# Performance work log

Measured on AMD Instinct MI355X. Metric: run time of the kernel, lower is better.

Reference implementation:

```python
import jax, jax.numpy as jnp
import numpy as np

N = 300000
MAX_TORSION = 7
MAX_RIGID = 8
MAX_SS = 3
MAX_ATOM = 24
NRES = 22
EPS = 1e-6


def v_norm_safe(v):
    # normalize last dim with epsilon clamp (torch v_norm_safe analogue)
    return v / jnp.clip(jnp.linalg.norm(v, axis=-1, keepdims=True), EPS)


def combine_operations(X, Y):
    # X, Y: [..., 4, 3] rigid ops (3x3 rotation rows + 1 translation row)
    rot = X[..., :3, :] @ Y[..., :3, :]
    t = jnp.einsum('...ij,...j->...i', X[..., :3, :], Y[..., 3, :]) + X[..., 3, :]
    return jnp.concatenate([rot, t[..., None, :]], axis=-2)


def setup_inputs() -> dict:
    key = jax.random.key(0)
    ks = jax.random.split(key, 9)
    return {
        'output_0': jax.random.normal(ks[0], (N, 2 * MAX_TORSION + MAX_SS, 1), jnp.float32),
        'output_1': jax.random.normal(ks[1], (N, 3, 3), jnp.float32),
        'pos': jax.random.normal(ks[2], (N, 3), jnp.float32),
        'ss': jax.random.randint(ks[3], (N,), 0, MAX_SS),
        'residue_type': jax.random.randint(ks[4], (N,), 0, NRES),
        'rigid_transforms': jax.random.normal(ks[5], (MAX_SS, NRES, MAX_RIGID, 4, 3), jnp.float32),
        'rigid_groups': jax.random.normal(ks[6], (MAX_SS, NRES, MAX_ATOM, 3), jnp.float32),
        'transforms_dep': jax.random.randint(ks[7], (NRES, MAX_RIGID), 0, MAX_RIGID),
        'rigids_dep': jax.random.randint(ks[8], (NRES, MAX_ATOM), 0, MAX_RIGID),
    }


def reference(output_0, output_1, pos, ss, residue_type,
              rigid_transforms, rigid_groups, transforms_dep, rigids_dep):
    # ---- StructureModule.output_to_opr_6D ----
    bb0 = output_1[:, :2]                                   # [N,2,3]
    e0 = v_norm_safe(bb0[:, 0])
    v1 = bb0[:, 1]
    u1 = v1 - e0 * jnp.sum(e0 * v1, axis=-1, keepdims=True)
    e1 = v_norm_safe(u1)
    e2 = jnp.cross(e0, e1)
    rot = jnp.stack([e0, e1, e2], axis=1).swapaxes(-1, -2)  # [N,3,3]
    t = 0.1 * output_1[:, 2][:, None, :]                    # [N,1,3]
    bb = jnp.concatenate([rot, t], axis=1)                  # [N,4,3]
    sc = v_norm_safe(output_0[:, :2 * MAX_TORSION].reshape(-1, MAX_TORSION, 2))

    # ---- build_structure ----
    transforms = rigid_transforms[ss, residue_type]         # [N,8,4,3]
    rigids = rigid_groups[ss, residue_type]                 # [N,24,3]
    tdep = transforms_dep[residue_type]                     # [N,8]
    rdep = rigids_dep[residue_type]                         # [N,24]

    n = output_0.shape[0]
    c, s = sc[..., 0], sc[..., 1]                           # [N,7]
    zr = jnp.zeros_like(c)
    on = jnp.ones_like(c)
    tor_rot = jnp.stack([
        jnp.stack([on, zr, zr], axis=-1),
        jnp.stack([zr, c, -s], axis=-1),
        jnp.stack([zr, s, c], axis=-1),
    ], axis=-2)                                             # [N,7,3,3]
    tor = jnp.concatenate(
        [tor_rot, jnp.zeros((n, MAX_TORSION, 1, 3), output_0.dtype)], axis=2)
    opr0 = jnp.concatenate([bb[:, :3], (bb[:, 3] + pos)[:, None]], axis=1)  # [N,4,3]
    opr = jnp.concatenate([opr0[:, None], tor], axis=1)     # [N,8,4,3]

    opr = combine_operations(transforms, opr)
    for i_tor in range(1, MAX_RIGID):                       # fixed 7-step dependency chain
        prev = jnp.take_along_axis(opr, tdep[:, i_tor][:, None, None, None], axis=1)[:, 0]
        opr = opr.at[:, i_tor].set(combine_operations(prev, opr[:, i_tor]))

    opr_g = jnp.take_along_axis(opr, rdep[:, :, None, None], axis=1)  # [N,24,4,3]
    R = jnp.einsum('naij,naj->nai', opr_g[:, :, :3], rigids) + opr_g[:, :, 3]
    return (R, opr[:, 0])
```

## Files before the change

### kernel.cpp

```cpp
#include <hip/hip_runtime.h>
#include <math.h>

#define NRES 22


__device__ __forceinline__ void sel8(const float (&fr)[8][12], int d, float (&P)[12]) {
    const bool b0 = (d & 1) != 0;
    const bool b1 = (d & 2) != 0;
    const bool b2 = (d & 4) != 0;
#pragma unroll
    for (int k = 0; k < 12; ++k) {
        float a01 = b0 ? fr[1][k] : fr[0][k];
        float a23 = b0 ? fr[3][k] : fr[2][k];
        float a45 = b0 ? fr[5][k] : fr[4][k];
        float a67 = b0 ? fr[7][k] : fr[6][k];
        float b03 = b1 ? a23 : a01;
        float b47 = b1 ? a67 : a45;
        P[k] = b2 ? b47 : b03;
    }
}

__device__ __forceinline__ void apply_point(const float (&F)[12], float x, float y, float z,
                                            float &px, float &py, float &pz) {
    px = fmaf(F[0], x, fmaf(F[1], y, fmaf(F[2], z, F[9])));
    py = fmaf(F[3], x, fmaf(F[4], y, fmaf(F[5], z, F[10])));
    pz = fmaf(F[6], x, fmaf(F[7], y, fmaf(F[8], z, F[11])));
}

extern "C" __global__ __launch_bounds__(256)
void model_kernel(const float* __restrict__ o0,
                  const float* __restrict__ o1,
                  const float* __restrict__ pos,
                  const int*   __restrict__ ssArr,
                  const int*   __restrict__ rtArr,
                  const float* __restrict__ rigT,
                  const float* __restrict__ rigG,
                  const int*   __restrict__ tdepArr,
                  const int*   __restrict__ rdepArr,
                  float* __restrict__ outR,
                  float* __restrict__ outF,
                  int N)
{
    const int tid0    = (int)blockIdx.x * 256 + (int)threadIdx.x;
    const int gstride = (int)gridDim.x * 256;

    for (int res = tid0; res < N; res += gstride) {
        const int s  = ssArr[res];
        const int rt = rtArr[res];

        float c[7], sn[7];
        const float* o0p = o0 + (size_t)res * 17;
#pragma unroll
        for (int t = 0; t < 7; ++t) {
            float cr = o0p[2 * t], sr = o0p[2 * t + 1];
            float n2 = cr * cr + sr * sr;
            float inv = rsqrtf(fmaxf(n2, 1e-12f));
            c[t]  = cr * inv;
            sn[t] = sr * inv;
        }

        const float* o1p = o1 + (size_t)res * 9;
        float r0x = o1p[0], r0y = o1p[1], r0z = o1p[2];
        float v1x = o1p[3], v1y = o1p[4], v1z = o1p[5];
        float t2x = o1p[6], t2y = o1p[7], t2z = o1p[8];
        float inv0 = rsqrtf(fmaxf(r0x * r0x + r0y * r0y + r0z * r0z, 1e-12f));
        float e0x = r0x * inv0, e0y = r0y * inv0, e0z = r0z * inv0;
        float d01 = e0x * v1x + e0y * v1y + e0z * v1z;
        float u1x = v1x - e0x * d01, u1y = v1y - e0y * d01, u1z = v1z - e0z * d01;
        float inv1 = rsqrtf(fmaxf(u1x * u1x + u1y * u1y + u1z * u1z, 1e-12f));
        float e1x = u1x * inv1, e1y = u1y * inv1, e1z = u1z * inv1;
        float e2x = e0y * e1z - e0z * e1y;
        float e2y = e0z * e1x - e0x * e1z;
        float e2z = e0x * e1y - e0y * e1x;
        const float* pp = pos + (size_t)res * 3;
        float btx = 0.1f * t2x + pp[0];
        float bty = 0.1f * t2y + pp[1];
        float btz = 0.1f * t2z + pp[2];

        const int sr22 = s * NRES + rt;
        const float4* T4 = (const float4*)rigT + (size_t)sr22 * 24;

        float fr[8][12];

        {
            float4 q0 = T4[0], q1 = T4[1], q2 = T4[2];
            float T0[12] = {q0.x, q0.y, q0.z, q0.w, q1.x, q1.y, q1.z, q1.w,
                            q2.x, q2.y, q2.z, q2.w};
#pragma unroll
            for (int i = 0; i < 3; ++i) {
                float a = T0[i * 3 + 0], b = T0[i * 3 + 1], d = T0[i * 3 + 2];
                fr[0][i * 3 + 0] = a * e0x + b * e0y + d * e0z;
                fr[0][i * 3 + 1] = a * e1x + b * e1y + d * e1z;
                fr[0][i * 3 + 2] = a * e2x + b * e2y + d * e2z;
                fr[0][9 + i]     = a * btx + b * bty + d * btz + T0[9 + i];
            }
        }

#pragma unroll
        for (int f = 1; f < 8; ++f) {
            float4 q0 = T4[f * 3 + 0], q1 = T4[f * 3 + 1], q2 = T4[f * 3 + 2];
            float Tf[12] = {q0.x, q0.y, q0.z, q0.w, q1.x, q1.y, q1.z, q1.w,
                            q2.x, q2.y, q2.z, q2.w};
            float cc = c[f - 1], ssn = sn[f - 1];
#pragma unroll
            for (int i = 0; i < 3; ++i) {
                fr[f][i * 3 + 0] = Tf[i * 3 + 0];
                fr[f][i * 3 + 1] = Tf[i * 3 + 1] * cc + Tf[i * 3 + 2] * ssn;
                fr[f][i * 3 + 2] = Tf[i * 3 + 2] * cc - Tf[i * 3 + 1] * ssn;
                fr[f][9 + i]     = Tf[9 + i];
            }
        }

        int tdv[8];
        {
            const int4* tdq = (const int4*)(tdepArr + rt * 8);
            int4 a = tdq[0], b = tdq[1];
            tdv[0] = a.x; tdv[1] = a.y; tdv[2] = a.z; tdv[3] = a.w;
            tdv[4] = b.x; tdv[5] = b.y; tdv[6] = b.z; tdv[7] = b.w;
        }
#pragma unroll
        for (int i = 1; i < 8; ++i) {
            float P[12];
            sel8(fr, tdv[i] & 7, P);
            float Y[12];
#pragma unroll
            for (int k = 0; k < 12; ++k) Y[k] = fr[i][k];
#pragma unroll
            for (int r = 0; r < 3; ++r) {
                float a = P[r * 3 + 0], b = P[r * 3 + 1], d = P[r * 3 + 2];
#pragma unroll
                for (int j = 0; j < 3; ++j)
                    fr[i][r * 3 + j] = a * Y[j] + b * Y[3 + j] + d * Y[6 + j];
                fr[i][9 + r] = a * Y[9] + b * Y[10] + d * Y[11] + P[9 + r];
            }
        }

        const float4* G4  = (const float4*)rigG + (size_t)sr22 * 18;
        const int4*   RD4 = (const int4*)(rdepArr + rt * 24);
        float4* OR4 = (float4*)(outR + (size_t)res * 72);
#pragma unroll
        for (int ck = 0; ck < 6; ++ck) {
            int4 rd = RD4[ck];
            float4 g0 = G4[ck * 3 + 0], g1 = G4[ck * 3 + 1], g2 = G4[ck * 3 + 2];
            float P[12];
            float p0x, p0y, p0z, p1x, p1y, p1z, p2x, p2y, p2z, p3x, p3y, p3z;
            sel8(fr, rd.x & 7, P); apply_point(P, g0.x, g0.y, g0.z, p0x, p0y, p0z);
            sel8(fr, rd.y & 7, P); apply_point(P, g0.w, g1.x, g1.y, p1x, p1y, p1z);
            sel8(fr, rd.z & 7, P); apply_point(P, g1.z, g1.w, g2.x, p2x, p2y, p2z);
            sel8(fr, rd.w & 7, P); apply_point(P, g2.y, g2.z, g2.w, p3x, p3y, p3z);
            OR4[ck * 3 + 0] = make_float4(p0x, p0y, p0z, p1x);
            OR4[ck * 3 + 1] = make_float4(p1y, p1z, p2x, p2y);
            OR4[ck * 3 + 2] = make_float4(p2z, p3x, p3y, p3z);
        }

        float4* OF4 = (float4*)(outF + (size_t)res * 12);
        OF4[0] = make_float4(fr[0][0], fr[0][1], fr[0][2], fr[0][3]);
        OF4[1] = make_float4(fr[0][4], fr[0][5], fr[0][6], fr[0][7]);
        OF4[2] = make_float4(fr[0][8], fr[0][9], fr[0][10], fr[0][11]);
    }
}

extern "C" void kernel_launch(void* const* d_in, const int* in_sizes, int n_in,
                              void* d_out, int out_size, void* d_ws, size_t ws_size,
                              hipStream_t stream) {
    const float* o0   = (const float*)d_in[0];
    const float* o1   = (const float*)d_in[1];
    const float* pos  = (const float*)d_in[2];
    const int*   ssA  = (const int*)d_in[3];
    const int*   rtA  = (const int*)d_in[4];
    const float* rigT = (const float*)d_in[5];
    const float* rigG = (const float*)d_in[6];
    const int*   tdep = (const int*)d_in[7];
    const int*   rdep = (const int*)d_in[8];

    const int N = in_sizes[3];
    float* outR = (float*)d_out;
    float* outF = (float*)d_out + (size_t)N * 72;

    int grid = (N + 255) / 256;
    if (grid > 1024) grid = 1024;
    model_kernel<<<grid, 256, 0, stream>>>(o0, o1, pos, ssA, rtA, rigT, rigG,
                                           tdep, rdep, outR, outF, N);
}
```

Baseline: 191.8 us.

## Stage rigid tables and dependency indices in padded shared memory per block

Each block now copies the rigid transform table, rigid group coordinates and both dependency index tables into LDS, with padded record strides chosen to reduce bank conflicts. The per-residue gathers then read from LDS instead of global/L2. The grid cap also drops from 1024 to 768 blocks so the preload is amortised over more residues per block. The cost is a prologue per block and about 49KB of LDS, which may limit occupancy.

```diff
diff --git a/kernel.cpp b/kernel.cpp
--- a/kernel.cpp
+++ b/kernel.cpp
@@ -3,6 +3,12 @@
 
 #define NRES 22
 
+#define ST_F    0
+#define SG_F    6600
+#define STD_I   11616
+#define SRD_I   11814
+#define TBL_F   12364
+#define SMEM_BYTES (TBL_F * 4)
 
 __device__ __forceinline__ void sel8(const float (&fr)[8][12], int d, float (&P)[12]) {
     const bool b0 = (d & 1) != 0;
@@ -41,7 +47,37 @@
                   float* __restrict__ outF,
                   int N)
 {
-    const int tid0    = (int)blockIdx.x * 256 + (int)threadIdx.x;
+    extern __shared__ __align__(16) float smem[];
+    int* smemI = (int*)smem;
+    const int tid = threadIdx.x;
+
+    {
+        const float4* s4 = (const float4*)rigT;
+        for (int t = tid; t < 1584; t += 256) {
+            float4 v = s4[t];
+            int rec = t / 24;
+            int k   = (t - rec * 24) << 2;
+            *(float4*)(smem + ST_F + rec * 100 + k) = v;
+        }
+    }
+    {
+        const float4* s4 = (const float4*)rigG;
+        for (int t = tid; t < 1188; t += 256) {
+            float4 v = s4[t];
+            int rec = t / 18;
+            int k   = (t - rec * 18) << 2;
+            *(float4*)(smem + SG_F + rec * 76 + k) = v;
+        }
+    }
+    for (int t = tid; t < 176; t += 256)
+        smemI[STD_I + (t >> 3) * 9 + (t & 7)] = tdepArr[t];
+    for (int t = tid; t < 528; t += 256) {
+        int r = t / 24;
+        smemI[SRD_I + r * 25 + (t - r * 24)] = rdepArr[t];
+    }
+    __syncthreads();
+
+    const int tid0    = (int)blockIdx.x * 256 + tid;
     const int gstride = (int)gridDim.x * 256;
 
     for (int res = tid0; res < N; res += gstride) {
@@ -53,8 +89,7 @@
 #pragma unroll
         for (int t = 0; t < 7; ++t) {
             float cr = o0p[2 * t], sr = o0p[2 * t + 1];
-            float n2 = cr * cr + sr * sr;
-            float inv = rsqrtf(fmaxf(n2, 1e-12f));
+            float inv = rsqrtf(fmaxf(cr * cr + sr * sr, 1e-12f));
             c[t]  = cr * inv;
             sn[t] = sr * inv;
         }
@@ -78,7 +113,7 @@
         float btz = 0.1f * t2z + pp[2];
 
         const int sr22 = s * NRES + rt;
-        const float4* T4 = (const float4*)rigT + (size_t)sr22 * 24;
+        const float4* T4 = (const float4*)smem + sr22 * 25;
 
         float fr[8][12];
 
@@ -111,17 +146,11 @@
             }
         }
 
-        int tdv[8];
-        {
-            const int4* tdq = (const int4*)(tdepArr + rt * 8);
-            int4 a = tdq[0], b = tdq[1];
-            tdv[0] = a.x; tdv[1] = a.y; tdv[2] = a.z; tdv[3] = a.w;
-            tdv[4] = b.x; tdv[5] = b.y; tdv[6] = b.z; tdv[7] = b.w;
-        }
+        const int* tdp = smemI + STD_I + rt * 9;
 #pragma unroll
         for (int i = 1; i < 8; ++i) {
             float P[12];
-            sel8(fr, tdv[i] & 7, P);
+            sel8(fr, tdp[i] & 7, P);
             float Y[12];
 #pragma unroll
             for (int k = 0; k < 12; ++k) Y[k] = fr[i][k];
@@ -135,19 +164,20 @@
             }
         }
 
-        const float4* G4  = (const float4*)rigG + (size_t)sr22 * 18;
-        const int4*   RD4 = (const int4*)(rdepArr + rt * 24);
+        const float4* G4  = (const float4*)smem + 1650 + sr22 * 19;
+        const int*    rdp = smemI + SRD_I + rt * 25;
         float4* OR4 = (float4*)(outR + (size_t)res * 72);
 #pragma unroll
         for (int ck = 0; ck < 6; ++ck) {
-            int4 rd = RD4[ck];
+            int d0 = rdp[ck * 4 + 0] & 7, d1 = rdp[ck * 4 + 1] & 7;
+            int d2 = rdp[ck * 4 + 2] & 7, d3 = rdp[ck * 4 + 3] & 7;
             float4 g0 = G4[ck * 3 + 0], g1 = G4[ck * 3 + 1], g2 = G4[ck * 3 + 2];
             float P[12];
             float p0x, p0y, p0z, p1x, p1y, p1z, p2x, p2y, p2z, p3x, p3y, p3z;
-            sel8(fr, rd.x & 7, P); apply_point(P, g0.x, g0.y, g0.z, p0x, p0y, p0z);
-            sel8(fr, rd.y & 7, P); apply_point(P, g0.w, g1.x, g1.y, p1x, p1y, p1z);
-            sel8(fr, rd.z & 7, P); apply_point(P, g1.z, g1.w, g2.x, p2x, p2y, p2z);
-            sel8(fr, rd.w & 7, P); apply_point(P, g2.y, g2.z, g2.w, p3x, p3y, p3z);
+            sel8(fr, d0, P); apply_point(P, g0.x, g0.y, g0.z, p0x, p0y, p0z);
+            sel8(fr, d1, P); apply_point(P, g0.w, g1.x, g1.y, p1x, p1y, p1z);
+            sel8(fr, d2, P); apply_point(P, g1.z, g1.w, g2.x, p2x, p2y, p2z);
+            sel8(fr, d3, P); apply_point(P, g2.y, g2.z, g2.w, p3x, p3y, p3z);
             OR4[ck * 3 + 0] = make_float4(p0x, p0y, p0z, p1x);
             OR4[ck * 3 + 1] = make_float4(p1y, p1z, p2x, p2y);
             OR4[ck * 3 + 2] = make_float4(p2z, p3x, p3y, p3z);
@@ -177,8 +207,15 @@
     float* outR = (float*)d_out;
     float* outF = (float*)d_out + (size_t)N * 72;
 
+    static bool attr_set = false;
+    if (!attr_set) {
+        hipFuncSetAttribute((const void*)model_kernel,
+                            hipFuncAttributeMaxDynamicSharedMemorySize, SMEM_BYTES);
+        attr_set = true;
+    }
+
     int grid = (N + 255) / 256;
-    if (grid > 1024) grid = 1024;
-    model_kernel<<<grid, 256, 0, stream>>>(o0, o1, pos, ssA, rtA, rigT, rigG,
-                                           tdep, rdep, outR, outF, N);
-}
+    if (grid > 768) grid = 768;
+    model_kernel<<<grid, 256, SMEM_BYTES, stream>>>(o0, o1, pos, ssA, rtA, rigT, rigG,
+                                                    tdep, rdep, outR, outF, N);
+}
```

New measurement: 185.3 us. 3.4% less time.
